# Optimization experiments

Measured on AMD Instinct MI355X. Metric: run time of the kernel, lower is better.

## Reference

```python
import jax, jax.numpy as jnp
import numpy as np

N_NODES = 100000
N_EDGES = 1600000
IN_CH = 128
HID = 64
OUT = 10
N_GRAPHS = 64


def gcn_conv(x, W, b, row, col, n):
    # PyG GCNConv: xw = x @ W; add self-loops (weight 1);
    # deg = scatter_add(weight, col); norm = d^-1/2[row] * d^-1/2[col];
    # out[col] += norm * xw[row]; out += b
    xw = x @ W  # [N, out_ch]
    loop = jnp.arange(n, dtype=row.dtype)
    r = jnp.concatenate([row, loop])
    c = jnp.concatenate([col, loop])
    deg = jax.ops.segment_sum(jnp.ones_like(c, dtype=xw.dtype), c, num_segments=n)
    dis = jnp.where(deg > 0, jax.lax.rsqrt(deg), 0.0)
    norm = dis[r] * dis[c]  # [E+N]
    msgs = norm[:, None] * xw[r]  # gather + scale
    agg = jax.ops.segment_sum(msgs, c, num_segments=n)  # scatter-add
    return agg + b


def global_mean_pool(x, batch, num_graphs):
    sums = jax.ops.segment_sum(x, batch, num_segments=num_graphs)
    cnt = jax.ops.segment_sum(jnp.ones((x.shape[0],), x.dtype), batch, num_segments=num_graphs)
    return sums / jnp.maximum(cnt, 1.0)[:, None]


def setup_inputs() -> dict:
    key = jax.random.key(0)
    ks = jax.random.split(key, 9)
    x = jax.random.normal(ks[0], (N_NODES, IN_CH), dtype=jnp.float32)
    edge_index = jax.random.randint(ks[1], (2, N_EDGES), 0, N_NODES, dtype=jnp.int64)
    batch = jnp.sort(jax.random.randint(ks[2], (N_NODES,), 0, N_GRAPHS, dtype=jnp.int64))
    def glorot(k, shape):
        lim = np.sqrt(6.0 / (shape[0] + shape[1]))
        return jax.random.uniform(k, shape, jnp.float32, -lim, lim)
    W1 = glorot(ks[3], (IN_CH, HID)); b1 = jnp.zeros((HID,), jnp.float32)
    W2 = glorot(ks[4], (HID, HID)); b2 = jnp.zeros((HID,), jnp.float32)
    Wl = glorot(ks[5], (HID, OUT)); bl = jnp.zeros((OUT,), jnp.float32)
    return {"x": x, "W1": W1, "b1": b1, "W2": W2, "b2": b2,
            "Wl": Wl, "bl": bl, "edge_index": edge_index, "batch": batch}


def reference(x, W1, b1, W2, b2, Wl, bl, edge_index, batch):
    row, col = edge_index[0], edge_index[1]
    n = x.shape[0]
    h = jax.nn.relu(gcn_conv(x, W1, b1, row, col, n))
    h = jax.nn.relu(gcn_conv(h, W2, b2, row, col, n))
    g = global_mean_pool(h, batch, N_GRAPHS)  # [G, HID]
    return g @ Wl + bl  # [G, OUT]
```

## Files before the change

### kernel.cpp

```cpp
#include <hip/hip_runtime.h>


static __device__ inline ushort f32_to_bf16_rne(float f) {
    uint32_t u = __float_as_uint(f);
    uint32_t r = (u + 0x7fffu + ((u >> 16) & 1u)) >> 16;
    return (ushort)r;
}

__global__ __launch_bounds__(256) void deg_kernel(const int* __restrict__ col,
                                                  int* __restrict__ deg, int E) {
    int e = blockIdx.x * 256 + threadIdx.x;
    if (e < E) atomicAdd(&deg[col[e]], 1);
}

__global__ __launch_bounds__(256) void dis_kernel(const int* __restrict__ deg,
                                                  float* __restrict__ dis, int n) {
    int i = blockIdx.x * 256 + threadIdx.x;
    if (i < n) dis[i] = rsqrtf((float)deg[i] + 1.0f);
}

__global__ __launch_bounds__(512) void block_sum_kernel(const int* __restrict__ deg,
                                                        int* __restrict__ bsums, int n) {
    __shared__ int sm[512];
    int i = blockIdx.x * 512 + threadIdx.x;
    sm[threadIdx.x] = (i < n) ? deg[i] : 0;
    __syncthreads();
    for (int s = 256; s > 0; s >>= 1) {
        if (threadIdx.x < s) sm[threadIdx.x] += sm[threadIdx.x + s];
        __syncthreads();
    }
    if (threadIdx.x == 0) bsums[blockIdx.x] = sm[0];
}

__global__ __launch_bounds__(256) void scan_bsums_kernel(int* __restrict__ bsums, int nb) {
    __shared__ int sm[256];
    int v = (threadIdx.x < nb) ? bsums[threadIdx.x] : 0;
    sm[threadIdx.x] = v;
    __syncthreads();
    for (int off = 1; off < 256; off <<= 1) {
        int t = (threadIdx.x >= off) ? sm[threadIdx.x - off] : 0;
        __syncthreads();
        sm[threadIdx.x] += t;
        __syncthreads();
    }
    if (threadIdx.x < nb) bsums[threadIdx.x] = sm[threadIdx.x] - v;
}

__global__ __launch_bounds__(512) void scan_write_kernel(const int* __restrict__ deg,
                                                         const int* __restrict__ bsums,
                                                         int* __restrict__ rowptr,
                                                         int n, int E) {
    __shared__ int sm[512];
    int i = blockIdx.x * 512 + threadIdx.x;
    int v = (i < n) ? deg[i] : 0;
    sm[threadIdx.x] = v;
    __syncthreads();
    for (int off = 1; off < 512; off <<= 1) {
        int t = (threadIdx.x >= off) ? sm[threadIdx.x - off] : 0;
        __syncthreads();
        sm[threadIdx.x] += t;
        __syncthreads();
    }
    if (i < n) rowptr[i] = bsums[blockIdx.x] + sm[threadIdx.x] - v;
    if (blockIdx.x == 0 && threadIdx.x == 0) rowptr[n] = E;
}

__global__ __launch_bounds__(256) void fill_csr_kernel(const int* __restrict__ row,
                                                       const int* __restrict__ col,
                                                       const float* __restrict__ dis,
                                                       const int* __restrict__ rowptr,
                                                       int* __restrict__ fill,
                                                       int2* __restrict__ csr, int E) {
    int e = blockIdx.x * 256 + threadIdx.x;
    if (e >= E) return;
    int r = row[e], c = col[e];
    int pos = rowptr[c] + atomicAdd(&fill[c], 1);
    csr[pos] = make_int2(r, __float_as_int(dis[r] * dis[c]));
}

template <int K>
__global__ __launch_bounds__(256) void gemm_tiled(const float* __restrict__ x,
                                                  const float* __restrict__ W,
                                                  ushort* __restrict__ out, int n) {
    __shared__ float As[32][64];
    __shared__ float Ws[32 * 64];
    const int tid = threadIdx.x;
    const int tr = tid >> 4;
    const int tc = tid & 15;
    const int base = blockIdx.x * 64;

    float acc[4][4];
#pragma unroll
    for (int i = 0; i < 4; ++i)
#pragma unroll
        for (int j = 0; j < 4; ++j) acc[i][j] = 0.0f;

    const int tnode = tid >> 3;
    const int tk4 = (tid & 7) * 4;

    for (int kc = 0; kc < K; kc += 32) {
        __syncthreads();
#pragma unroll
        for (int h = 0; h < 2; ++h) {
            int m = tnode + h * 32;
            int node = base + m;
            float4 v = make_float4(0.f, 0.f, 0.f, 0.f);
            if (node < n) v = *(const float4*)&x[(size_t)node * K + kc + tk4];
            As[tk4 + 0][m] = v.x; As[tk4 + 1][m] = v.y;
            As[tk4 + 2][m] = v.z; As[tk4 + 3][m] = v.w;
        }
#pragma unroll
        for (int r = 0; r < 2; ++r) {
            int o = tid * 4 + r * 1024;
            *(float4*)&Ws[o] = *(const float4*)&W[kc * 64 + o];
        }
        __syncthreads();
#pragma unroll
        for (int k = 0; k < 32; ++k) {
            float4 a = *(const float4*)&As[k][tr * 4];
            float4 b = *(const float4*)&Ws[k * 64 + tc * 4];
            const float av[4] = {a.x, a.y, a.z, a.w};
            const float bv[4] = {b.x, b.y, b.z, b.w};
#pragma unroll
            for (int i = 0; i < 4; ++i)
#pragma unroll
                for (int j = 0; j < 4; ++j)
                    acc[i][j] = fmaf(av[i], bv[j], acc[i][j]);
        }
    }
#pragma unroll
    for (int i = 0; i < 4; ++i) {
        int node = base + tr * 4 + i;
        if (node < n) {
            ushort4 st;
            st.x = f32_to_bf16_rne(acc[i][0]);
            st.y = f32_to_bf16_rne(acc[i][1]);
            st.z = f32_to_bf16_rne(acc[i][2]);
            st.w = f32_to_bf16_rne(acc[i][3]);
            *(ushort4*)&out[(size_t)node * 64 + tc * 4] = st;
        }
    }
}

template <int OUT_BF16>
__global__ __launch_bounds__(256) void gcn_pull_kernel(const ushort* __restrict__ xw,
                                                       const int2* __restrict__ csr,
                                                       const int* __restrict__ rowptr,
                                                       const float* __restrict__ dis,
                                                       const float* __restrict__ b,
                                                       void* __restrict__ outv, int n) {
    const int lane = threadIdx.x & 63;
    const int wid = threadIdx.x >> 6;
    const int half = lane >> 5;
    const int q = lane & 31;
    const float2 bb = ((const float2*)b)[q];

    for (int i = blockIdx.x * 4 + wid; i < n; i += gridDim.x * 4) {
        int s = rowptr[i], t = rowptr[i + 1];
        float ax = 0.0f, ay = 0.0f;
        if (half == 0) {
            float di = dis[i];
            uint32_t u = *(const uint32_t*)(xw + ((size_t)i << 6) + (q << 1));
            float w = di * di;
            ax = w * __uint_as_float(u << 16);
            ay = w * __uint_as_float(u & 0xffff0000u);
        }
        int e = s + half;
        for (; e + 2 < t; e += 4) {
            int2 p0 = csr[e];
            int2 p1 = csr[e + 2];
            uint32_t u0 = *(const uint32_t*)(xw + ((size_t)p0.x << 6) + (q << 1));
            uint32_t u1 = *(const uint32_t*)(xw + ((size_t)p1.x << 6) + (q << 1));
            float n0 = __int_as_float(p0.y), n1 = __int_as_float(p1.y);
            ax = fmaf(n0, __uint_as_float(u0 << 16), ax);
            ay = fmaf(n0, __uint_as_float(u0 & 0xffff0000u), ay);
            ax = fmaf(n1, __uint_as_float(u1 << 16), ax);
            ay = fmaf(n1, __uint_as_float(u1 & 0xffff0000u), ay);
        }
        for (; e < t; e += 2) {
            int2 p = csr[e];
            uint32_t u = *(const uint32_t*)(xw + ((size_t)p.x << 6) + (q << 1));
            float nr = __int_as_float(p.y);
            ax = fmaf(nr, __uint_as_float(u << 16), ax);
            ay = fmaf(nr, __uint_as_float(u & 0xffff0000u), ay);
        }
        ax += __shfl_xor(ax, 32);
        ay += __shfl_xor(ay, 32);
        if (half == 0) {
            float v0 = fmaxf(ax + bb.x, 0.0f);
            float v1 = fmaxf(ay + bb.y, 0.0f);
            if (OUT_BF16) {
                ushort2 st = make_ushort2(f32_to_bf16_rne(v0), f32_to_bf16_rne(v1));
                *(ushort2*)((ushort*)outv + ((size_t)i << 6) + (q << 1)) = st;
            } else {
                *(float2*)((float*)outv + ((size_t)i << 6) + (q << 1)) = make_float2(v0, v1);
            }
        }
    }
}

__global__ __launch_bounds__(256) void pool_kernel(const ushort* __restrict__ h,
                                                   const int* __restrict__ batch,
                                                   float* __restrict__ pool,
                                                   float* __restrict__ cnt, int n) {
    const int lane = threadIdx.x & 63;
    const int wid = threadIdx.x >> 6;
    const int start = (blockIdx.x * 4 + wid) * 256;
    const int end = min(start + 256, n);
    if (start >= end) return;
    int gcur = batch[start];
    float acc = 0.0f;
    int c = 0;
    for (int i = start; i < end; ++i) {
        int g = batch[i];
        if (g != gcur) {
            atomicAdd(&pool[gcur * 64 + lane], acc);
            if (lane == 0) atomicAdd(&cnt[gcur], (float)c);
            acc = 0.0f; c = 0; gcur = g;
        }
        acc += __uint_as_float((uint32_t)h[(size_t)i * 64 + lane] << 16);
        ++c;
    }
    atomicAdd(&pool[gcur * 64 + lane], acc);
    if (lane == 0) atomicAdd(&cnt[gcur], (float)c);
}

__global__ __launch_bounds__(640) void final_kernel(const float* __restrict__ pool,
                                                    const float* __restrict__ cnt,
                                                    const float* __restrict__ Wl,
                                                    const float* __restrict__ bl,
                                                    float* __restrict__ out) {
    int tid = threadIdx.x;
    int g = tid / 10, o = tid % 10;
    float inv = 1.0f / fmaxf(cnt[g], 1.0f);
    float acc = 0.0f;
#pragma unroll
    for (int l = 0; l < 64; ++l)
        acc = fmaf(pool[g * 64 + l] * inv, Wl[l * 10 + o], acc);
    out[tid] = acc + bl[o];
}

extern "C" void kernel_launch(void* const* d_in, const int* in_sizes, int n_in,
                              void* d_out, int out_size, void* d_ws, size_t ws_size,
                              hipStream_t stream) {
    const float* x  = (const float*)d_in[0];
    const float* W1 = (const float*)d_in[1];
    const float* b1 = (const float*)d_in[2];
    const float* W2 = (const float*)d_in[3];
    const float* b2 = (const float*)d_in[4];
    const float* Wl = (const float*)d_in[5];
    const float* bl = (const float*)d_in[6];
    const int*   ei = (const int*)d_in[7];
    const int*   batch = (const int*)d_in[8];
    float* out = (float*)d_out;

    const int n = in_sizes[8];
    const int E = in_sizes[7] / 2;
    const int F = 64;

    const int* row = ei;
    const int* col = ei + E;

    char* p = (char*)d_ws;
    auto alloc = [&](size_t bytes) {
        char* r = p;
        p += (bytes + 255) & ~(size_t)255;
        return r;
    };
    int*    degi   = (int*)   alloc((size_t)n * 4);
    int*    rowptr = (int*)   alloc((size_t)(n + 1) * 4);
    int*    bsums  = (int*)   alloc(256 * 4);
    float*  dis    = (float*) alloc((size_t)n * 4);
    int2*   csr    = (int2*)  alloc((size_t)E * 8);
    ushort* xwB    = (ushort*)alloc((size_t)n * F * 2);
    float*  B      = (float*) alloc((size_t)n * F * 4);
    float*  pool   = (float*) alloc(64 * 64 * 4);
    float*  cnt    = (float*) alloc(64 * 4);

    const int nb_edge = (E + 255) / 256;
    const int nb_node = (n + 255) / 256;
    const int nb_scan = (n + 511) / 512;
    const int nb_gemm = (n + 63) / 64;

    hipMemsetAsync(degi, 0, (size_t)n * 4, stream);
    deg_kernel<<<nb_edge, 256, 0, stream>>>(col, degi, E);
    block_sum_kernel<<<nb_scan, 512, 0, stream>>>(degi, bsums, n);
    scan_bsums_kernel<<<1, 256, 0, stream>>>(bsums, nb_scan);
    scan_write_kernel<<<nb_scan, 512, 0, stream>>>(degi, bsums, rowptr, n, E);
    dis_kernel<<<nb_node, 256, 0, stream>>>(degi, dis, n);
    hipMemsetAsync(degi, 0, (size_t)n * 4, stream);
    fill_csr_kernel<<<nb_edge, 256, 0, stream>>>(row, col, dis, rowptr, degi, csr, E);

    gemm_tiled<128><<<nb_gemm, 256, 0, stream>>>(x, W1, xwB, n);
    gcn_pull_kernel<0><<<2048, 256, 0, stream>>>(xwB, csr, rowptr, dis, b1, B, n);

    gemm_tiled<64><<<nb_gemm, 256, 0, stream>>>(B, W2, xwB, n);
    gcn_pull_kernel<1><<<2048, 256, 0, stream>>>(xwB, csr, rowptr, dis, b2, B, n);

    hipMemsetAsync(pool, 0, (64 * 64 + 64) * sizeof(float), stream);
    pool_kernel<<<(n + 1023) / 1024, 256, 0, stream>>>((const ushort*)B, batch, pool, cnt, n);
    final_kernel<<<1, 640, 0, stream>>>(pool, cnt, Wl, bl, out);
}
```

Before: 496.9 us.

## Replace full CSR build with bucketed binning and LDS-atomic aggregation

Swaps the per-node CSR construction (degree scan plus atomic fill) for a two-level bucket sort. Edges are grouped into 256-node destination buckets and packed as a 20-bit source plus an 8-bit local destination, and aggregation is done with shared-memory float atomics per bucket. The dis[src] factor is folded into the GEMM epilogue, so edges no longer carry a norm. Layer 1 now writes bf16, the second GEMM reads bf16, and pooling uses finer work chunks. The cost is many LDS atomics and only about 391 aggregation blocks, which may underfill the GPU, and the 20-bit source packing limits the node count.

```diff
diff --git a/kernel.cpp b/kernel.cpp
--- a/kernel.cpp
+++ b/kernel.cpp
@@ -1,16 +1,33 @@
 #include <hip/hip_runtime.h>
 
+
+#define NBLK 256
+#define MAXNB 512
 
 static __device__ inline ushort f32_to_bf16_rne(float f) {
     uint32_t u = __float_as_uint(f);
     uint32_t r = (u + 0x7fffu + ((u >> 16) & 1u)) >> 16;
     return (ushort)r;
 }
-
-__global__ __launch_bounds__(256) void deg_kernel(const int* __restrict__ col,
-                                                  int* __restrict__ deg, int E) {
-    int e = blockIdx.x * 256 + threadIdx.x;
-    if (e < E) atomicAdd(&deg[col[e]], 1);
+static __device__ inline float bf_lo(uint32_t u) { return __uint_as_float(u << 16); }
+static __device__ inline float bf_hi(uint32_t u) { return __uint_as_float(u & 0xffff0000u); }
+
+__global__ __launch_bounds__(256) void hist_kernel(const int* __restrict__ col,
+                                                   int* __restrict__ deg,
+                                                   int* __restrict__ hist,
+                                                   int E, int NB, int C) {
+    __shared__ int cnt[MAXNB];
+    for (int i = threadIdx.x; i < NB; i += 256) cnt[i] = 0;
+    __syncthreads();
+    const int b = blockIdx.x;
+    const int e1 = min(b * C + C, E);
+    for (int e = b * C + threadIdx.x; e < e1; e += 256) {
+        int c = col[e];
+        atomicAdd(&cnt[c >> 8], 1);
+        atomicAdd(&deg[c], 1);
+    }
+    __syncthreads();
+    for (int i = threadIdx.x; i < NB; i += 256) hist[b * NB + i] = cnt[i];
 }
 
 __global__ __launch_bounds__(256) void dis_kernel(const int* __restrict__ deg,
@@ -19,22 +36,12 @@
     if (i < n) dis[i] = rsqrtf((float)deg[i] + 1.0f);
 }
 
-__global__ __launch_bounds__(512) void block_sum_kernel(const int* __restrict__ deg,
-                                                        int* __restrict__ bsums, int n) {
-    __shared__ int sm[512];
-    int i = blockIdx.x * 512 + threadIdx.x;
-    sm[threadIdx.x] = (i < n) ? deg[i] : 0;
-    __syncthreads();
-    for (int s = 256; s > 0; s >>= 1) {
-        if (threadIdx.x < s) sm[threadIdx.x] += sm[threadIdx.x + s];
-        __syncthreads();
-    }
-    if (threadIdx.x == 0) bsums[blockIdx.x] = sm[0];
-}
-
-__global__ __launch_bounds__(256) void scan_bsums_kernel(int* __restrict__ bsums, int nb) {
+__global__ __launch_bounds__(256) void scan_bucket_kernel(int* __restrict__ hist,
+                                                          int* __restrict__ total,
+                                                          int NB) {
     __shared__ int sm[256];
-    int v = (threadIdx.x < nb) ? bsums[threadIdx.x] : 0;
+    const int k = blockIdx.x;
+    int v = hist[threadIdx.x * NB + k];
     sm[threadIdx.x] = v;
     __syncthreads();
     for (int off = 1; off < 256; off <<= 1) {
@@ -43,16 +50,15 @@
         sm[threadIdx.x] += t;
         __syncthreads();
     }
-    if (threadIdx.x < nb) bsums[threadIdx.x] = sm[threadIdx.x] - v;
-}
-
-__global__ __launch_bounds__(512) void scan_write_kernel(const int* __restrict__ deg,
-                                                         const int* __restrict__ bsums,
-                                                         int* __restrict__ rowptr,
-                                                         int n, int E) {
+    hist[threadIdx.x * NB + k] = sm[threadIdx.x] - v;
+    if (threadIdx.x == 255) total[k] = sm[255];
+}
+
+__global__ __launch_bounds__(512) void start_scan_kernel(const int* __restrict__ total,
+                                                         int* __restrict__ start,
+                                                         int NB, int E) {
     __shared__ int sm[512];
-    int i = blockIdx.x * 512 + threadIdx.x;
-    int v = (i < n) ? deg[i] : 0;
+    int v = (threadIdx.x < NB) ? total[threadIdx.x] : 0;
     sm[threadIdx.x] = v;
     __syncthreads();
     for (int off = 1; off < 512; off <<= 1) {
@@ -61,28 +67,39 @@
         sm[threadIdx.x] += t;
         __syncthreads();
     }
-    if (i < n) rowptr[i] = bsums[blockIdx.x] + sm[threadIdx.x] - v;
-    if (blockIdx.x == 0 && threadIdx.x == 0) rowptr[n] = E;
-}
-
-__global__ __launch_bounds__(256) void fill_csr_kernel(const int* __restrict__ row,
+    if (threadIdx.x < NB) start[threadIdx.x] = sm[threadIdx.x] - v;
+    if (threadIdx.x == 0) start[NB] = E;
+}
+
+__global__ __launch_bounds__(256) void fill_bin_kernel(const int* __restrict__ row,
                                                        const int* __restrict__ col,
-                                                       const float* __restrict__ dis,
-                                                       const int* __restrict__ rowptr,
-                                                       int* __restrict__ fill,
-                                                       int2* __restrict__ csr, int E) {
-    int e = blockIdx.x * 256 + threadIdx.x;
-    if (e >= E) return;
-    int r = row[e], c = col[e];
-    int pos = rowptr[c] + atomicAdd(&fill[c], 1);
-    csr[pos] = make_int2(r, __float_as_int(dis[r] * dis[c]));
-}
-
-template <int K>
-__global__ __launch_bounds__(256) void gemm_tiled(const float* __restrict__ x,
+                                                       const int* __restrict__ hist,
+                                                       const int* __restrict__ start,
+                                                       int* __restrict__ inter,
+                                                       int E, int NB, int C) {
+    __shared__ int sbase[MAXNB];
+    __shared__ int lcnt[MAXNB];
+    const int b = blockIdx.x;
+    for (int i = threadIdx.x; i < NB; i += 256) {
+        sbase[i] = start[i] + hist[b * NB + i];
+        lcnt[i] = 0;
+    }
+    __syncthreads();
+    const int e1 = min(b * C + C, E);
+    for (int e = b * C + threadIdx.x; e < e1; e += 256) {
+        int r = row[e], c = col[e];
+        int k = c >> 8;
+        int idx = atomicAdd(&lcnt[k], 1);
+        inter[sbase[k] + idx] = r | ((c & 255) << 20);
+    }
+}
+
+template <int K, bool BF16IN>
+__global__ __launch_bounds__(256) void gemm_tiled(const void* __restrict__ xin,
                                                   const float* __restrict__ W,
+                                                  const float* __restrict__ dis,
                                                   ushort* __restrict__ out, int n) {
-    __shared__ float As[32][64];
+    __shared__ float As[32][68];
     __shared__ float Ws[32 * 64];
     const int tid = threadIdx.x;
     const int tr = tid >> 4;
@@ -104,10 +121,20 @@
         for (int h = 0; h < 2; ++h) {
             int m = tnode + h * 32;
             int node = base + m;
-            float4 v = make_float4(0.f, 0.f, 0.f, 0.f);
-            if (node < n) v = *(const float4*)&x[(size_t)node * K + kc + tk4];
-            As[tk4 + 0][m] = v.x; As[tk4 + 1][m] = v.y;
-            As[tk4 + 2][m] = v.z; As[tk4 + 3][m] = v.w;
+            float f0 = 0.f, f1 = 0.f, f2 = 0.f, f3 = 0.f;
+            if (node < n) {
+                if (BF16IN) {
+                    const ushort* xb = (const ushort*)xin;
+                    uint2 v = *(const uint2*)(xb + (size_t)node * K + kc + tk4);
+                    f0 = bf_lo(v.x); f1 = bf_hi(v.x); f2 = bf_lo(v.y); f3 = bf_hi(v.y);
+                } else {
+                    const float* xf = (const float*)xin;
+                    float4 v = *(const float4*)&xf[(size_t)node * K + kc + tk4];
+                    f0 = v.x; f1 = v.y; f2 = v.z; f3 = v.w;
+                }
+            }
+            As[tk4 + 0][m] = f0; As[tk4 + 1][m] = f1;
+            As[tk4 + 2][m] = f2; As[tk4 + 3][m] = f3;
         }
 #pragma unroll
         for (int r = 0; r < 2; ++r) {
@@ -132,69 +159,102 @@
     for (int i = 0; i < 4; ++i) {
         int node = base + tr * 4 + i;
         if (node < n) {
+            float d = dis[node];
             ushort4 st;
-            st.x = f32_to_bf16_rne(acc[i][0]);
-            st.y = f32_to_bf16_rne(acc[i][1]);
-            st.z = f32_to_bf16_rne(acc[i][2]);
-            st.w = f32_to_bf16_rne(acc[i][3]);
+            st.x = f32_to_bf16_rne(acc[i][0] * d);
+            st.y = f32_to_bf16_rne(acc[i][1] * d);
+            st.z = f32_to_bf16_rne(acc[i][2] * d);
+            st.w = f32_to_bf16_rne(acc[i][3] * d);
             *(ushort4*)&out[(size_t)node * 64 + tc * 4] = st;
         }
     }
 }
 
-template <int OUT_BF16>
-__global__ __launch_bounds__(256) void gcn_pull_kernel(const ushort* __restrict__ xw,
-                                                       const int2* __restrict__ csr,
-                                                       const int* __restrict__ rowptr,
-                                                       const float* __restrict__ dis,
-                                                       const float* __restrict__ b,
-                                                       void* __restrict__ outv, int n) {
-    const int lane = threadIdx.x & 63;
-    const int wid = threadIdx.x >> 6;
-    const int half = lane >> 5;
-    const int q = lane & 31;
-    const float2 bb = ((const float2*)b)[q];
-
-    for (int i = blockIdx.x * 4 + wid; i < n; i += gridDim.x * 4) {
-        int s = rowptr[i], t = rowptr[i + 1];
-        float ax = 0.0f, ay = 0.0f;
-        if (half == 0) {
-            float di = dis[i];
-            uint32_t u = *(const uint32_t*)(xw + ((size_t)i << 6) + (q << 1));
-            float w = di * di;
-            ax = w * __uint_as_float(u << 16);
-            ay = w * __uint_as_float(u & 0xffff0000u);
-        }
-        int e = s + half;
-        for (; e + 2 < t; e += 4) {
-            int2 p0 = csr[e];
-            int2 p1 = csr[e + 2];
-            uint32_t u0 = *(const uint32_t*)(xw + ((size_t)p0.x << 6) + (q << 1));
-            uint32_t u1 = *(const uint32_t*)(xw + ((size_t)p1.x << 6) + (q << 1));
-            float n0 = __int_as_float(p0.y), n1 = __int_as_float(p1.y);
-            ax = fmaf(n0, __uint_as_float(u0 << 16), ax);
-            ay = fmaf(n0, __uint_as_float(u0 & 0xffff0000u), ay);
-            ax = fmaf(n1, __uint_as_float(u1 << 16), ax);
-            ay = fmaf(n1, __uint_as_float(u1 & 0xffff0000u), ay);
-        }
-        for (; e < t; e += 2) {
-            int2 p = csr[e];
-            uint32_t u = *(const uint32_t*)(xw + ((size_t)p.x << 6) + (q << 1));
-            float nr = __int_as_float(p.y);
-            ax = fmaf(nr, __uint_as_float(u << 16), ax);
-            ay = fmaf(nr, __uint_as_float(u & 0xffff0000u), ay);
-        }
-        ax += __shfl_xor(ax, 32);
-        ay += __shfl_xor(ay, 32);
-        if (half == 0) {
-            float v0 = fmaxf(ax + bb.x, 0.0f);
-            float v1 = fmaxf(ay + bb.y, 0.0f);
-            if (OUT_BF16) {
-                ushort2 st = make_ushort2(f32_to_bf16_rne(v0), f32_to_bf16_rne(v1));
-                *(ushort2*)((ushort*)outv + ((size_t)i << 6) + (q << 1)) = st;
-            } else {
-                *(float2*)((float*)outv + ((size_t)i << 6) + (q << 1)) = make_float2(v0, v1);
-            }
+#define PAD 65
+__global__ __launch_bounds__(256) void gcn_pull_lds(const ushort* __restrict__ xws,
+                                                    const int* __restrict__ inter,
+                                                    const int* __restrict__ start,
+                                                    const float* __restrict__ dis,
+                                                    const float* __restrict__ bias,
+                                                    ushort* __restrict__ outb, int n) {
+    __shared__ float acc[256 * PAD];
+    const int tid = threadIdx.x;
+    for (int i = tid; i < 256 * PAD; i += 256) acc[i] = 0.0f;
+    __syncthreads();
+    const int bkt = blockIdx.x;
+    const int s = start[bkt], t = start[bkt + 1];
+    const int tq = tid & 3, eq = tid >> 2;
+    const int chb = tq << 4;
+
+    int e = s + eq;
+    for (; e + 64 < t; e += 128) {
+        int w0 = inter[e], w1 = inter[e + 64];
+        int s0 = w0 & 0xFFFFF, s1 = w1 & 0xFFFFF;
+        int d0 = (int)(((unsigned)w0) >> 20), d1 = (int)(((unsigned)w1) >> 20);
+        const uint4* r0 = (const uint4*)(xws + ((size_t)s0 << 6));
+        const uint4* r1 = (const uint4*)(xws + ((size_t)s1 << 6));
+        uint4 a0 = r0[tq * 2], b0 = r0[tq * 2 + 1];
+        uint4 a1 = r1[tq * 2], b1 = r1[tq * 2 + 1];
+        float* A0 = &acc[d0 * PAD + chb];
+        atomicAdd(A0 + 0,  bf_lo(a0.x)); atomicAdd(A0 + 1,  bf_hi(a0.x));
+        atomicAdd(A0 + 2,  bf_lo(a0.y)); atomicAdd(A0 + 3,  bf_hi(a0.y));
+        atomicAdd(A0 + 4,  bf_lo(a0.z)); atomicAdd(A0 + 5,  bf_hi(a0.z));
+        atomicAdd(A0 + 6,  bf_lo(a0.w)); atomicAdd(A0 + 7,  bf_hi(a0.w));
+        atomicAdd(A0 + 8,  bf_lo(b0.x)); atomicAdd(A0 + 9,  bf_hi(b0.x));
+        atomicAdd(A0 + 10, bf_lo(b0.y)); atomicAdd(A0 + 11, bf_hi(b0.y));
+        atomicAdd(A0 + 12, bf_lo(b0.z)); atomicAdd(A0 + 13, bf_hi(b0.z));
+        atomicAdd(A0 + 14, bf_lo(b0.w)); atomicAdd(A0 + 15, bf_hi(b0.w));
+        float* A1 = &acc[d1 * PAD + chb];
+        atomicAdd(A1 + 0,  bf_lo(a1.x)); atomicAdd(A1 + 1,  bf_hi(a1.x));
+        atomicAdd(A1 + 2,  bf_lo(a1.y)); atomicAdd(A1 + 3,  bf_hi(a1.y));
+        atomicAdd(A1 + 4,  bf_lo(a1.z)); atomicAdd(A1 + 5,  bf_hi(a1.z));
+        atomicAdd(A1 + 6,  bf_lo(a1.w)); atomicAdd(A1 + 7,  bf_hi(a1.w));
+        atomicAdd(A1 + 8,  bf_lo(b1.x)); atomicAdd(A1 + 9,  bf_hi(b1.x));
+        atomicAdd(A1 + 10, bf_lo(b1.y)); atomicAdd(A1 + 11, bf_hi(b1.y));
+        atomicAdd(A1 + 12, bf_lo(b1.z)); atomicAdd(A1 + 13, bf_hi(b1.z));
+        atomicAdd(A1 + 14, bf_lo(b1.w)); atomicAdd(A1 + 15, bf_hi(b1.w));
+    }
+    for (; e < t; e += 64) {
+        int w0 = inter[e];
+        int s0 = w0 & 0xFFFFF;
+        int d0 = (int)(((unsigned)w0) >> 20);
+        const uint4* r0 = (const uint4*)(xws + ((size_t)s0 << 6));
+        uint4 a0 = r0[tq * 2], b0 = r0[tq * 2 + 1];
+        float* A0 = &acc[d0 * PAD + chb];
+        atomicAdd(A0 + 0,  bf_lo(a0.x)); atomicAdd(A0 + 1,  bf_hi(a0.x));
+        atomicAdd(A0 + 2,  bf_lo(a0.y)); atomicAdd(A0 + 3,  bf_hi(a0.y));
+        atomicAdd(A0 + 4,  bf_lo(a0.z)); atomicAdd(A0 + 5,  bf_hi(a0.z));
+        atomicAdd(A0 + 6,  bf_lo(a0.w)); atomicAdd(A0 + 7,  bf_hi(a0.w));
+        atomicAdd(A0 + 8,  bf_lo(b0.x)); atomicAdd(A0 + 9,  bf_hi(b0.x));
+        atomicAdd(A0 + 10, bf_lo(b0.y)); atomicAdd(A0 + 11, bf_hi(b0.y));
+        atomicAdd(A0 + 12, bf_lo(b0.z)); atomicAdd(A0 + 13, bf_hi(b0.z));
+        atomicAdd(A0 + 14, bf_lo(b0.w)); atomicAdd(A0 + 15, bf_hi(b0.w));
+    }
+    __syncthreads();
+    const int node = (bkt << 8) + tid;
+    if (node < n) {
+        const float di = dis[node];
+        const uint4* rp = (const uint4*)(xws + ((size_t)node << 6));
+        const float* ab = &acc[tid * PAD];
+        ushort* op = outb + ((size_t)node << 6);
+#pragma unroll
+        for (int j = 0; j < 8; ++j) {
+            uint4 v = rp[j];
+            const int c0 = j * 8;
+            float o0 = fmaxf(fmaf(di, ab[c0 + 0] + bf_lo(v.x), bias[c0 + 0]), 0.f);
+            float o1 = fmaxf(fmaf(di, ab[c0 + 1] + bf_hi(v.x), bias[c0 + 1]), 0.f);
+            float o2 = fmaxf(fmaf(di, ab[c0 + 2] + bf_lo(v.y), bias[c0 + 2]), 0.f);
+            float o3 = fmaxf(fmaf(di, ab[c0 + 3] + bf_hi(v.y), bias[c0 + 3]), 0.f);
+            float o4 = fmaxf(fmaf(di, ab[c0 + 4] + bf_lo(v.z), bias[c0 + 4]), 0.f);
+            float o5 = fmaxf(fmaf(di, ab[c0 + 5] + bf_hi(v.z), bias[c0 + 5]), 0.f);
+            float o6 = fmaxf(fmaf(di, ab[c0 + 6] + bf_lo(v.w), bias[c0 + 6]), 0.f);
+            float o7 = fmaxf(fmaf(di, ab[c0 + 7] + bf_hi(v.w), bias[c0 + 7]), 0.f);
+            uint4 sv;
+            sv.x = (uint32_t)f32_to_bf16_rne(o0) | ((uint32_t)f32_to_bf16_rne(o1) << 16);
+            sv.y = (uint32_t)f32_to_bf16_rne(o2) | ((uint32_t)f32_to_bf16_rne(o3) << 16);
+            sv.z = (uint32_t)f32_to_bf16_rne(o4) | ((uint32_t)f32_to_bf16_rne(o5) << 16);
+            sv.w = (uint32_t)f32_to_bf16_rne(o6) | ((uint32_t)f32_to_bf16_rne(o7) << 16);
+            *(uint4*)(op + c0) = sv;
         }
     }
 }
@@ -205,13 +265,13 @@
                                                    float* __restrict__ cnt, int n) {
     const int lane = threadIdx.x & 63;
     const int wid = threadIdx.x >> 6;
-    const int start = (blockIdx.x * 4 + wid) * 256;
-    const int end = min(start + 256, n);
-    if (start >= end) return;
-    int gcur = batch[start];
+    const int startn = (blockIdx.x * 4 + wid) * 32;
+    const int endn = min(startn + 32, n);
+    if (startn >= endn) return;
+    int gcur = batch[startn];
     float acc = 0.0f;
     int c = 0;
-    for (int i = start; i < end; ++i) {
+    for (int i = startn; i < endn; ++i) {
         int g = batch[i];
         if (g != gcur) {
             atomicAdd(&pool[gcur * 64 + lane], acc);
@@ -261,43 +321,42 @@
     const int* row = ei;
     const int* col = ei + E;
 
+    const int NB = (n + 255) >> 8;
+    const int C  = (E + NBLK - 1) / NBLK;
+
     char* p = (char*)d_ws;
     auto alloc = [&](size_t bytes) {
         char* r = p;
         p += (bytes + 255) & ~(size_t)255;
         return r;
     };
-    int*    degi   = (int*)   alloc((size_t)n * 4);
-    int*    rowptr = (int*)   alloc((size_t)(n + 1) * 4);
-    int*    bsums  = (int*)   alloc(256 * 4);
-    float*  dis    = (float*) alloc((size_t)n * 4);
-    int2*   csr    = (int2*)  alloc((size_t)E * 8);
-    ushort* xwB    = (ushort*)alloc((size_t)n * F * 2);
-    float*  B      = (float*) alloc((size_t)n * F * 4);
-    float*  pool   = (float*) alloc(64 * 64 * 4);
-    float*  cnt    = (float*) alloc(64 * 4);
-
-    const int nb_edge = (E + 255) / 256;
-    const int nb_node = (n + 255) / 256;
-    const int nb_scan = (n + 511) / 512;
+    int*    degi  = (int*)   alloc((size_t)n * 4);
+    float*  dis   = (float*) alloc((size_t)n * 4);
+    int*    hist  = (int*)   alloc((size_t)NBLK * MAXNB * 4);
+    int*    total = (int*)   alloc(MAXNB * 4);
+    int*    startp= (int*)   alloc((MAXNB + 1) * 4);
+    int*    inter = (int*)   alloc((size_t)E * 4);
+    ushort* xws   = (ushort*)alloc((size_t)n * F * 2);
+    ushort* B16   = (ushort*)alloc((size_t)n * F * 2);
+    float*  pool  = (float*) alloc(64 * 64 * 4);
+    float*  cnt   = (float*) alloc(64 * 4);
+
     const int nb_gemm = (n + 63) / 64;
 
     hipMemsetAsync(degi, 0, (size_t)n * 4, stream);
-    deg_kernel<<<nb_edge, 256, 0, stream>>>(col, degi, E);
-    block_sum_kernel<<<nb_scan, 512, 0, stream>>>(degi, bsums, n);
-    scan_bsums_kernel<<<1, 256, 0, stream>>>(bsums, nb_scan);
-    scan_write_kernel<<<nb_scan, 512, 0, stream>>>(degi, bsums, rowptr, n, E);
-    dis_kernel<<<nb_node, 256, 0, stream>>>(degi, dis, n);
-    hipMemsetAsync(degi, 0, (size_t)n * 4, stream);
-    fill_csr_kernel<<<nb_edge, 256, 0, stream>>>(row, col, dis, rowptr, degi, csr, E);
-
-    gemm_tiled<128><<<nb_gemm, 256, 0, stream>>>(x, W1, xwB, n);
-    gcn_pull_kernel<0><<<2048, 256, 0, stream>>>(xwB, csr, rowptr, dis, b1, B, n);
-
-    gemm_tiled<64><<<nb_gemm, 256, 0, stream>>>(B, W2, xwB, n);
-    gcn_pull_kernel<1><<<2048, 256, 0, stream>>>(xwB, csr, rowptr, dis, b2, B, n);
+    hist_kernel<<<NBLK, 256, 0, stream>>>(col, degi, hist, E, NB, C);
+    scan_bucket_kernel<<<NB, 256, 0, stream>>>(hist, total, NB);
+    start_scan_kernel<<<1, 512, 0, stream>>>(total, startp, NB, E);
+    dis_kernel<<<(n + 255) / 256, 256, 0, stream>>>(degi, dis, n);
+    fill_bin_kernel<<<NBLK, 256, 0, stream>>>(row, col, hist, startp, inter, E, NB, C);
+
+    gemm_tiled<128, false><<<nb_gemm, 256, 0, stream>>>(x, W1, dis, xws, n);
+    gcn_pull_lds<<<NB, 256, 0, stream>>>(xws, inter, startp, dis, b1, B16, n);
+
+    gemm_tiled<64, true><<<nb_gemm, 256, 0, stream>>>(B16, W2, dis, xws, n);
+    gcn_pull_lds<<<NB, 256, 0, stream>>>(xws, inter, startp, dis, b2, B16, n);
 
     hipMemsetAsync(pool, 0, (64 * 64 + 64) * sizeof(float), stream);
-    pool_kernel<<<(n + 1023) / 1024, 256, 0, stream>>>((const ushort*)B, batch, pool, cnt, n);
+    pool_kernel<<<(n + 127) / 128, 256, 0, stream>>>(B16, batch, pool, cnt, n);
     final_kernel<<<1, 640, 0, stream>>>(pool, cnt, Wl, bl, out);
 }
```

Measured after the change: 1.633 ms. 229% more time.
